# Optimization experiments

Measured on AMD Instinct MI355X. Metric: run time of the kernel, lower is better.

Reference implementation:

```python
import jax, jax.numpy as jnp
import numpy as np

B, T, C, K, TNEI = 16, 1024, 1024, 8, 2
H = int(C * 1.5)  # FeedForward hidden = int(1.5*in_dim)
EPS = 1e-5


def setup_inputs() -> dict:
    key = jax.random.key(0)
    ks = jax.random.split(key, 16)
    ws = C ** -0.5  # fan-in style init scale for projections
    return {
        "x": jax.random.normal(ks[0], (B, T, C), jnp.float32),
        "radj": jax.random.uniform(ks[1], (B, T, K), jnp.float32),
        "inxs": jax.random.randint(ks[2], (B, T, K), 0, T),
        "Wq": jax.random.normal(ks[3], (C, C), jnp.float32) * ws,
        "Wk": jax.random.normal(ks[4], (C, C), jnp.float32) * ws,
        "Wv": jax.random.normal(ks[5], (C, C), jnp.float32) * ws,
        "Wo": jax.random.normal(ks[6], (C, C), jnp.float32) * ws,
        "ln1_g": jnp.ones((C,), jnp.float32),
        "ln1_b": jnp.zeros((C,), jnp.float32),
        "W1": jax.random.normal(ks[7], (C, H), jnp.float32) * ws,
        "b1": jnp.zeros((H,), jnp.float32),
        "W2": jax.random.normal(ks[8], (H, C), jnp.float32) * (H ** -0.5),
        "b2": jnp.zeros((C,), jnp.float32),
        "ln2_g": jnp.ones((C,), jnp.float32),
        "ln2_b": jnp.zeros((C,), jnp.float32),
    }


def _layernorm(x, g, b):
    mu = jnp.mean(x, axis=-1, keepdims=True)
    var = jnp.mean(jnp.square(x - mu), axis=-1, keepdims=True)
    return (x - mu) * jax.lax.rsqrt(var + EPS) * g + b


def reference(x, radj, inxs, Wq, Wk, Wv, Wo, ln1_g, ln1_b, W1, b1, W2, b2, ln2_g, ln2_b):
    scale = 1.0 / jnp.sqrt(jnp.asarray(C, x.dtype))
    gather = jax.vmap(lambda a, i: a[i])  # (T,C),(T,K) -> (T,K,C), vmapped over B

    # MBasicReason: tnei hops of top-k neighbor attention (adjacency-biased)
    h = x
    for _ in range(TNEI):
        q = h @ Wq                                  # (B,T,C)
        kn = gather(h @ Wk, inxs)                   # (B,T,K,C)
        vn = gather(h @ Wv, inxs)                   # (B,T,K,C)
        scores = jnp.einsum('btc,btkc->btk', q, kn) * scale + radj
        attn = jax.nn.softmax(scores, axis=-1)      # (B,T,K); dropout off (eval)
        h = jnp.einsum('btk,btkc->btc', attn, vn) @ Wo

    # residual + LN, FFN, residual + LN
    y = _layernorm(x + jax.nn.relu(h), ln1_g, ln1_b)
    f = jax.nn.relu(y @ W1 + b1) @ W2 + b2
    return _layernorm(y + f, ln2_g, ln2_b)
```

## Files before the change

### kernel.cpp

```cpp
#include <hip/hip_runtime.h>
#include <hip/hip_bf16.h>
#include <cstddef>
#include <cstdint>

#define B_    16
#define T_    1024
#define C_    1024
#define K_    8
#define H_    1536
#define TNEI_ 2
static constexpr float EPS_ = 1e-5f;

typedef __attribute__((ext_vector_type(8))) short bf16x8;
typedef __attribute__((ext_vector_type(4))) float f32x4;

__device__ __forceinline__ float bf2f(unsigned short u) {
    return __uint_as_float(((unsigned)u) << 16);
}
__device__ __forceinline__ unsigned short f2bf(float f) {
    __hip_bfloat16 h = __float2bfloat16(f);
    union { __hip_bfloat16 h; unsigned short u; } cvt;
    cvt.h = h;
    return cvt.u;
}

__device__ __forceinline__ void gload_lds16(const void* g, void* l) {
    __builtin_amdgcn_global_load_lds(
        (const __attribute__((address_space(1))) void*)g,
        (__attribute__((address_space(3))) void*)l,
        16, 0, 0);
}

#define VMCNT0 asm volatile("s_waitcnt vmcnt(0)" ::: "memory")
#define VMCNT4 asm volatile("s_waitcnt vmcnt(4)" ::: "memory")
#define BARRIER do {                                   \
    __builtin_amdgcn_sched_barrier(0);                 \
    __builtin_amdgcn_s_barrier();                      \
    asm volatile("" ::: "memory");                     \
    __builtin_amdgcn_sched_barrier(0);                 \
} while (0)

__global__ __launch_bounds__(256) void f2bf_kernel(
    const float* __restrict__ in, unsigned short* __restrict__ out)
{
    const size_t i = (size_t)blockIdx.x * 256 + threadIdx.x;
    const float4 v = *reinterpret_cast<const float4*>(&in[i * 4]);
    ushort4 o;
    o.x = f2bf(v.x); o.y = f2bf(v.y); o.z = f2bf(v.z); o.w = f2bf(v.w);
    *reinterpret_cast<ushort4*>(&out[i * 4]) = o;
}

__global__ __launch_bounds__(256) void wtrans_kernel(
    const float* __restrict__ W, unsigned short* __restrict__ WT, int R, int Cc)
{
    __shared__ float t[32][33];
    const int c0 = blockIdx.x * 32, r0 = blockIdx.y * 32;
    const int tx = threadIdx.x & 31, ty = threadIdx.x >> 5;
    #pragma unroll
    for (int i = 0; i < 4; ++i)
        t[ty + 8 * i][tx] = W[(size_t)(r0 + ty + 8 * i) * Cc + c0 + tx];
    __syncthreads();
    #pragma unroll
    for (int i = 0; i < 4; ++i)
        WT[(size_t)(c0 + ty + 8 * i) * R + r0 + tx] = f2bf(t[tx][ty + 8 * i]);
}

template <int OUT_BF16, int BIAS, int RELU>
__global__ __launch_bounds__(256, 2) void gemm_bt_kernel(
    const unsigned short* __restrict__ A, const unsigned short* __restrict__ Bt,
    const float* __restrict__ bias, void* __restrict__ Cout,
    int M, int N, int K)
{
    constexpr int BK = 32;
    __shared__ unsigned short smem[3 * 8192];

    const int tid  = threadIdx.x;
    const int lane = tid & 63;
    const int wid  = tid >> 6;
    const int wm   = wid >> 1, wn = wid & 1;

    const int nwg  = gridDim.x * gridDim.y;
    int bidl = blockIdx.y * gridDim.x + blockIdx.x;
    bidl = (bidl & 7) * (nwg >> 3) + (bidl >> 3);
    const int bx = bidl % gridDim.x;
    const int by = bidl / gridDim.x;
    const int row0 = by * 128;
    const int col0 = bx * 128;

    const int NT = K >> 5;

    const int sub = lane >> 2;
    const int kk  = (((lane & 3) ^ ((lane >> 3) & 3))) * 8;

    f32x4 acc[4][4] = {};

    auto stage = [&](int kt, int bufi) {
        unsigned short* As = smem + bufi * 8192;
        unsigned short* Bs = As + 4096;
        #pragma unroll
        for (int i = 0; i < 2; ++i) {
            const int chunk = i * 4 + wid;
            const int r = chunk * 16 + sub;
            gload_lds16(&A[(size_t)(row0 + r) * K + kt + kk], &As[chunk * 512]);
        }
        #pragma unroll
        for (int i = 0; i < 2; ++i) {
            const int chunk = i * 4 + wid;
            const int r = chunk * 16 + sub;
            gload_lds16(&Bt[(size_t)(col0 + r) * K + kt + kk], &Bs[chunk * 512]);
        }
    };

    const int slot = ((lane >> 4) ^ ((lane >> 1) & 3)) * 8;
    auto loadfrag = [&](int bufi, bf16x8* a, bf16x8* b) {
        const unsigned short* As = smem + bufi * 8192;
        const unsigned short* Bs = As + 4096;
        #pragma unroll
        for (int m = 0; m < 4; ++m) {
            const int r = wm * 64 + m * 16 + (lane & 15);
            a[m] = *reinterpret_cast<const bf16x8*>(&As[r * 32 + slot]);
        }
        #pragma unroll
        for (int n = 0; n < 4; ++n) {
            const int c = wn * 64 + n * 16 + (lane & 15);
            b[n] = *reinterpret_cast<const bf16x8*>(&Bs[c * 32 + slot]);
        }
    };

    auto mfma16 = [&](const bf16x8* a, const bf16x8* b) {
        __builtin_amdgcn_s_setprio(1);
        #pragma unroll
        for (int m = 0; m < 4; ++m)
            #pragma unroll
            for (int n = 0; n < 4; ++n)
                acc[m][n] = __builtin_amdgcn_mfma_f32_16x16x32_bf16(
                    a[m], b[n], acc[m][n], 0, 0, 0);
        __builtin_amdgcn_s_setprio(0);
    };

    bf16x8 fa[4], fb[4];

    stage(0, 0);
    stage(BK, 1);
    VMCNT4;
    BARRIER;
    loadfrag(0, fa, fb);

    int bs = 2, br = 1;
    for (int t = 0; t < NT; ++t) {
        if (t + 2 < NT) stage((t + 2) * BK, bs);
        if (++bs == 3) bs = 0;
        mfma16(fa, fb);
        if (t + 1 < NT) {
            if (t + 2 < NT) { VMCNT4; } else { VMCNT0; }
            BARRIER;
            loadfrag(br, fa, fb);
        }
        if (++br == 3) br = 0;
    }

    if (OUT_BF16) {
        __syncthreads();
        char* tile = (char*)smem;
        #pragma unroll
        for (int m = 0; m < 4; ++m) {
            #pragma unroll
            for (int n = 0; n < 4; ++n) {
                const int cc = wn * 64 + n * 16 + (lane & 15);
                const float bv = BIAS ? bias[col0 + cc] : 0.0f;
                #pragma unroll
                for (int r = 0; r < 4; ++r) {
                    const int rr = wm * 64 + m * 16 + (lane >> 4) * 4 + r;
                    float v = acc[m][n][r] + bv;
                    if (RELU) v = fmaxf(v, 0.0f);
                    const int byte = (rr * 256 + cc * 2) ^ (((rr >> 2) & 3) << 5);
                    *reinterpret_cast<unsigned short*>(tile + byte) = f2bf(v);
                }
            }
        }
        __syncthreads();
        const int cchunk = tid & 15;
        const int rloc   = tid >> 4;
        #pragma unroll
        for (int p = 0; p < 8; ++p) {
            const int rr = p * 16 + rloc;
            const int byte = (rr * 256 + cchunk * 16) ^ (((rr >> 2) & 3) << 5);
            const uint4 v = *reinterpret_cast<const uint4*>(tile + byte);
            *reinterpret_cast<uint4*>(
                &((unsigned short*)Cout)[(size_t)(row0 + rr) * N + col0 + cchunk * 8]) = v;
        }
    } else {
        #pragma unroll
        for (int m = 0; m < 4; ++m) {
            #pragma unroll
            for (int n = 0; n < 4; ++n) {
                const int cg = col0 + wn * 64 + n * 16 + (lane & 15);
                const float bv = BIAS ? bias[cg] : 0.0f;
                #pragma unroll
                for (int r = 0; r < 4; ++r) {
                    const int rg = row0 + wm * 64 + m * 16 + (lane >> 4) * 4 + r;
                    float v = acc[m][n][r] + bv;
                    if (RELU) v = fmaxf(v, 0.0f);
                    ((float*)Cout)[(size_t)rg * N + cg] = v;
                }
            }
        }
    }
}

__global__ __launch_bounds__(256) void attn_kernel(
    const unsigned short* __restrict__ qkv, const int* __restrict__ inxs,
    const float* __restrict__ radj, unsigned short* __restrict__ out)
{
    const int bt  = blockIdx.x;
    const int b   = bt >> 10;
    const int tid = threadIdx.x;
    const float scale = 0.03125f;

    __shared__ int   s_idx[K_];
    __shared__ float s_sc[K_];
    __shared__ float red[K_][4];

    if (tid < K_) s_idx[tid] = inxs[bt * K_ + tid];
    __syncthreads();

    const ushort4 qv = *reinterpret_cast<const ushort4*>(
        &qkv[(size_t)bt * 3072 + tid * 4]);
    const float qf[4] = { bf2f(qv.x), bf2f(qv.y), bf2f(qv.z), bf2f(qv.w) };

    float part[K_];
    #pragma unroll
    for (int k = 0; k < K_; ++k) {
        const size_t nb = (size_t)b * T_ + s_idx[k];
        const ushort4 kv = *reinterpret_cast<const ushort4*>(
            &qkv[nb * 3072 + 1024 + tid * 4]);
        part[k] = qf[0] * bf2f(kv.x) + qf[1] * bf2f(kv.y)
                + qf[2] * bf2f(kv.z) + qf[3] * bf2f(kv.w);
    }

    const int lane = tid & 63, wid = tid >> 6;
    #pragma unroll
    for (int k = 0; k < K_; ++k) {
        float v = part[k];
        #pragma unroll
        for (int off = 32; off; off >>= 1) v += __shfl_xor(v, off);
        if (lane == 0) red[k][wid] = v;
    }
    __syncthreads();
    if (tid < K_) {
        s_sc[tid] = (red[tid][0] + red[tid][1] + red[tid][2] + red[tid][3]) * scale
                    + radj[bt * K_ + tid];
    }
    __syncthreads();

    float m = s_sc[0];
    #pragma unroll
    for (int k = 1; k < K_; ++k) m = fmaxf(m, s_sc[k]);
    float w[K_], wsum = 0.f;
    #pragma unroll
    for (int k = 0; k < K_; ++k) { w[k] = expf(s_sc[k] - m); wsum += w[k]; }
    const float inv = 1.0f / wsum;

    float o[4] = {0.f, 0.f, 0.f, 0.f};
    #pragma unroll
    for (int k = 0; k < K_; ++k) {
        const size_t nb = (size_t)b * T_ + s_idx[k];
        const ushort4 vv = *reinterpret_cast<const ushort4*>(
            &qkv[nb * 3072 + 2048 + tid * 4]);
        const float wk = w[k] * inv;
        o[0] = fmaf(wk, bf2f(vv.x), o[0]);
        o[1] = fmaf(wk, bf2f(vv.y), o[1]);
        o[2] = fmaf(wk, bf2f(vv.z), o[2]);
        o[3] = fmaf(wk, bf2f(vv.w), o[3]);
    }
    ushort4 ov;
    ov.x = f2bf(o[0]); ov.y = f2bf(o[1]); ov.z = f2bf(o[2]); ov.w = f2bf(o[3]);
    *reinterpret_cast<ushort4*>(&out[(size_t)bt * C_ + tid * 4]) = ov;
}

template <int RELU, int WB>
__global__ __launch_bounds__(256) void ln_residual_kernel(
    const float* __restrict__ a, const float* __restrict__ bb,
    const float* __restrict__ g, const float* __restrict__ beta,
    float* __restrict__ out, unsigned short* __restrict__ outb)
{
    const int bt  = blockIdx.x;
    const int tid = threadIdx.x;

    const float4 av = *reinterpret_cast<const float4*>(&a[(size_t)bt * C_ + tid * 4]);
    const float4 bv = *reinterpret_cast<const float4*>(&bb[(size_t)bt * C_ + tid * 4]);
    float4 s;
    s.x = av.x + (RELU ? fmaxf(bv.x, 0.f) : bv.x);
    s.y = av.y + (RELU ? fmaxf(bv.y, 0.f) : bv.y);
    s.z = av.z + (RELU ? fmaxf(bv.z, 0.f) : bv.z);
    s.w = av.w + (RELU ? fmaxf(bv.w, 0.f) : bv.w);

    float sum = s.x + s.y + s.z + s.w;
    float sq  = s.x * s.x + s.y * s.y + s.z * s.z + s.w * s.w;

    const int lane = tid & 63, wid = tid >> 6;
    __shared__ float rs[4], rq[4];
    #pragma unroll
    for (int off = 32; off; off >>= 1) {
        sum += __shfl_xor(sum, off);
        sq  += __shfl_xor(sq,  off);
    }
    if (lane == 0) { rs[wid] = sum; rq[wid] = sq; }
    __syncthreads();
    sum = rs[0] + rs[1] + rs[2] + rs[3];
    sq  = rq[0] + rq[1] + rq[2] + rq[3];

    const float mu  = sum * (1.0f / C_);
    const float var = sq * (1.0f / C_) - mu * mu;
    const float r   = rsqrtf(var + EPS_);

    const float4 gv = *reinterpret_cast<const float4*>(&g[tid * 4]);
    const float4 be = *reinterpret_cast<const float4*>(&beta[tid * 4]);
    float4 o;
    o.x = (s.x - mu) * r * gv.x + be.x;
    o.y = (s.y - mu) * r * gv.y + be.y;
    o.z = (s.z - mu) * r * gv.z + be.z;
    o.w = (s.w - mu) * r * gv.w + be.w;
    *reinterpret_cast<float4*>(&out[(size_t)bt * C_ + tid * 4]) = o;
    if (WB) {
        ushort4 ob;
        ob.x = f2bf(o.x); ob.y = f2bf(o.y); ob.z = f2bf(o.z); ob.w = f2bf(o.w);
        *reinterpret_cast<ushort4*>(&outb[(size_t)bt * C_ + tid * 4]) = ob;
    }
}

extern "C" void kernel_launch(void* const* d_in, const int* in_sizes, int n_in,
                              void* d_out, int out_size, void* d_ws, size_t ws_size,
                              hipStream_t stream)
{
    const float* x     = (const float*)d_in[0];
    const float* radj  = (const float*)d_in[1];
    const int*   inxs  = (const int*)  d_in[2];
    const float* Wq    = (const float*)d_in[3];
    const float* Wk    = (const float*)d_in[4];
    const float* Wv    = (const float*)d_in[5];
    const float* Wo    = (const float*)d_in[6];
    const float* ln1_g = (const float*)d_in[7];
    const float* ln1_b = (const float*)d_in[8];
    const float* W1    = (const float*)d_in[9];
    const float* b1    = (const float*)d_in[10];
    const float* W2    = (const float*)d_in[11];
    const float* b2    = (const float*)d_in[12];
    const float* ln2_g = (const float*)d_in[13];
    const float* ln2_b = (const float*)d_in[14];
    float* out = (float*)d_out;

    char* wsb = (char*)d_ws;
    const size_t MB = 1 << 20;
    unsigned short* WqkvT = (unsigned short*)(wsb + 0 * MB);
    unsigned short* WoT   = (unsigned short*)(wsb + 6 * MB);
    unsigned short* W1T   = (unsigned short*)(wsb + 8 * MB);
    unsigned short* W2T   = (unsigned short*)(wsb + 11 * MB);
    unsigned short* xb  = (unsigned short*)(wsb + 16 * MB);
    unsigned short* hb  = xb;
    unsigned short* qkv = (unsigned short*)(wsb + 48 * MB);
    unsigned short* ab  = (unsigned short*)(wsb + 144 * MB);
    float*          h2  = (float*)(wsb + 48 * MB);
    float*          y   = (float*)(wsb + 112 * MB);
    unsigned short* yb  = (unsigned short*)(wsb + 176 * MB);
    unsigned short* hid = (unsigned short*)(wsb + 208 * MB);
    float*          f   = (float*)(wsb + 48 * MB);

    const int M = B_ * T_;
    const dim3 blk(256);
    const dim3 gQKV(3 * C_ / 128, M / 128);
    const dim3 gC(C_ / 128, M / 128);
    const dim3 gH(H_ / 128, M / 128);

    wtrans_kernel<<<dim3(32, 32), blk, 0, stream>>>(Wq, WqkvT,                C_, C_);
    wtrans_kernel<<<dim3(32, 32), blk, 0, stream>>>(Wk, WqkvT + 1024 * 1024,  C_, C_);
    wtrans_kernel<<<dim3(32, 32), blk, 0, stream>>>(Wv, WqkvT + 2048 * 1024,  C_, C_);
    wtrans_kernel<<<dim3(32, 32), blk, 0, stream>>>(Wo, WoT, C_, C_);
    wtrans_kernel<<<dim3(48, 32), blk, 0, stream>>>(W1, W1T, C_, H_);
    wtrans_kernel<<<dim3(32, 48), blk, 0, stream>>>(W2, W2T, H_, C_);
    f2bf_kernel<<<dim3((size_t)M * C_ / 1024), blk, 0, stream>>>(x, xb);

    for (int hop = 0; hop < TNEI_; ++hop) {
        const unsigned short* hin = (hop == 0) ? xb : hb;
        gemm_bt_kernel<1, 0, 0><<<gQKV, blk, 0, stream>>>(hin, WqkvT, nullptr, qkv,
                                                          M, 3 * C_, C_);
        attn_kernel<<<dim3(M), blk, 0, stream>>>(qkv, inxs, radj, ab);
        if (hop == 0)
            gemm_bt_kernel<1, 0, 0><<<gC, blk, 0, stream>>>(ab, WoT, nullptr, hb,
                                                            M, C_, C_);
        else
            gemm_bt_kernel<0, 0, 0><<<gC, blk, 0, stream>>>(ab, WoT, nullptr, h2,
                                                            M, C_, C_);
    }

    ln_residual_kernel<1, 1><<<dim3(M), blk, 0, stream>>>(x, h2, ln1_g, ln1_b, y, yb);
    gemm_bt_kernel<1, 1, 1><<<gH, blk, 0, stream>>>(yb,  W1T, b1, hid, M, H_, C_);
    gemm_bt_kernel<0, 1, 0><<<gC, blk, 0, stream>>>(hid, W2T, b2, f,   M, C_, H_);
    ln_residual_kernel<0, 0><<<dim3(M), blk, 0, stream>>>(y, f, ln2_g, ln2_b, out, nullptr);
}
```

Baseline: 801.8 us.

## Enlarge GEMM tiles to 256x256 with 512-thread workgroups

Doubles the GEMM macro-tile in both dimensions to 256x256 and uses 8 waves per workgroup, each computing a 128x64 sub-tile with twice the accumulators. The bf16 epilogue is reorganised into two passes through LDS so the larger output tile fits the staging buffer. The goal is higher arithmetic intensity and fewer global loads per FLOP. The costs are more registers per thread, larger LDS use, and fewer workgroups, for example only 256 for the C-wide GEMMs, which may hurt occupancy and load balance across CUs.

```diff
diff --git a/kernel.cpp b/kernel.cpp
--- a/kernel.cpp
+++ b/kernel.cpp
@@ -66,58 +66,58 @@
 }
 
 template <int OUT_BF16, int BIAS, int RELU>
-__global__ __launch_bounds__(256, 2) void gemm_bt_kernel(
+__global__ __launch_bounds__(512, 2) void gemm_bt_kernel(
     const unsigned short* __restrict__ A, const unsigned short* __restrict__ Bt,
     const float* __restrict__ bias, void* __restrict__ Cout,
     int M, int N, int K)
 {
     constexpr int BK = 32;
-    __shared__ unsigned short smem[3 * 8192];
+    __shared__ unsigned short smem[3 * 16384];
 
     const int tid  = threadIdx.x;
     const int lane = tid & 63;
     const int wid  = tid >> 6;
-    const int wm   = wid >> 1, wn = wid & 1;
+    const int wm   = wid >> 2, wn = wid & 3;
 
     const int nwg  = gridDim.x * gridDim.y;
     int bidl = blockIdx.y * gridDim.x + blockIdx.x;
     bidl = (bidl & 7) * (nwg >> 3) + (bidl >> 3);
     const int bx = bidl % gridDim.x;
     const int by = bidl / gridDim.x;
-    const int row0 = by * 128;
-    const int col0 = bx * 128;
+    const int row0 = by * 256;
+    const int col0 = bx * 256;
 
     const int NT = K >> 5;
 
     const int sub = lane >> 2;
     const int kk  = (((lane & 3) ^ ((lane >> 3) & 3))) * 8;
 
-    f32x4 acc[4][4] = {};
+    f32x4 acc[8][4] = {};
 
     auto stage = [&](int kt, int bufi) {
-        unsigned short* As = smem + bufi * 8192;
-        unsigned short* Bs = As + 4096;
+        unsigned short* As = smem + bufi * 16384;
+        unsigned short* Bs = As + 8192;
         #pragma unroll
         for (int i = 0; i < 2; ++i) {
-            const int chunk = i * 4 + wid;
-            const int r = chunk * 16 + sub;
-            gload_lds16(&A[(size_t)(row0 + r) * K + kt + kk], &As[chunk * 512]);
+            const int cg = i * 8 + wid;
+            const int r = cg * 16 + sub;
+            gload_lds16(&A[(size_t)(row0 + r) * K + kt + kk], &As[cg * 512]);
         }
         #pragma unroll
         for (int i = 0; i < 2; ++i) {
-            const int chunk = i * 4 + wid;
-            const int r = chunk * 16 + sub;
-            gload_lds16(&Bt[(size_t)(col0 + r) * K + kt + kk], &Bs[chunk * 512]);
+            const int cg = i * 8 + wid;
+            const int r = cg * 16 + sub;
+            gload_lds16(&Bt[(size_t)(col0 + r) * K + kt + kk], &Bs[cg * 512]);
         }
     };
 
     const int slot = ((lane >> 4) ^ ((lane >> 1) & 3)) * 8;
     auto loadfrag = [&](int bufi, bf16x8* a, bf16x8* b) {
-        const unsigned short* As = smem + bufi * 8192;
-        const unsigned short* Bs = As + 4096;
-        #pragma unroll
-        for (int m = 0; m < 4; ++m) {
-            const int r = wm * 64 + m * 16 + (lane & 15);
+        const unsigned short* As = smem + bufi * 16384;
+        const unsigned short* Bs = As + 8192;
+        #pragma unroll
+        for (int m = 0; m < 8; ++m) {
+            const int r = wm * 128 + m * 16 + (lane & 15);
             a[m] = *reinterpret_cast<const bf16x8*>(&As[r * 32 + slot]);
         }
         #pragma unroll
@@ -127,10 +127,10 @@
         }
     };
 
-    auto mfma16 = [&](const bf16x8* a, const bf16x8* b) {
+    auto mfma32 = [&](const bf16x8* a, const bf16x8* b) {
         __builtin_amdgcn_s_setprio(1);
         #pragma unroll
-        for (int m = 0; m < 4; ++m)
+        for (int m = 0; m < 8; ++m)
             #pragma unroll
             for (int n = 0; n < 4; ++n)
                 acc[m][n] = __builtin_amdgcn_mfma_f32_16x16x32_bf16(
@@ -138,7 +138,7 @@
         __builtin_amdgcn_s_setprio(0);
     };
 
-    bf16x8 fa[4], fb[4];
+    bf16x8 fa[8], fb[4];
 
     stage(0, 0);
     stage(BK, 1);
@@ -150,7 +150,7 @@
     for (int t = 0; t < NT; ++t) {
         if (t + 2 < NT) stage((t + 2) * BK, bs);
         if (++bs == 3) bs = 0;
-        mfma16(fa, fb);
+        mfma32(fa, fb);
         if (t + 1 < NT) {
             if (t + 2 < NT) { VMCNT4; } else { VMCNT0; }
             BARRIER;
@@ -160,45 +160,50 @@
     }
 
     if (OUT_BF16) {
-        __syncthreads();
         char* tile = (char*)smem;
         #pragma unroll
-        for (int m = 0; m < 4; ++m) {
+        for (int p = 0; p < 2; ++p) {
+            __syncthreads();
             #pragma unroll
-            for (int n = 0; n < 4; ++n) {
-                const int cc = wn * 64 + n * 16 + (lane & 15);
-                const float bv = BIAS ? bias[col0 + cc] : 0.0f;
+            for (int m4 = 0; m4 < 4; ++m4) {
+                const int m = p * 4 + m4;
                 #pragma unroll
-                for (int r = 0; r < 4; ++r) {
-                    const int rr = wm * 64 + m * 16 + (lane >> 4) * 4 + r;
-                    float v = acc[m][n][r] + bv;
-                    if (RELU) v = fmaxf(v, 0.0f);
-                    const int byte = (rr * 256 + cc * 2) ^ (((rr >> 2) & 3) << 5);
-                    *reinterpret_cast<unsigned short*>(tile + byte) = f2bf(v);
+                for (int n = 0; n < 4; ++n) {
+                    const int cc = wn * 64 + n * 16 + (lane & 15);
+                    const float bv = BIAS ? bias[col0 + cc] : 0.0f;
+                    #pragma unroll
+                    for (int r = 0; r < 4; ++r) {
+                        const int lrow = wm * 64 + m4 * 16 + (lane >> 4) * 4 + r;
+                        float v = acc[m][n][r] + bv;
+                        if (RELU) v = fmaxf(v, 0.0f);
+                        const int byte = (lrow * 512 + cc * 2) ^ (((lrow >> 2) & 3) << 5);
+                        *reinterpret_cast<unsigned short*>(tile + byte) = f2bf(v);
+                    }
                 }
             }
-        }
-        __syncthreads();
-        const int cchunk = tid & 15;
-        const int rloc   = tid >> 4;
-        #pragma unroll
-        for (int p = 0; p < 8; ++p) {
-            const int rr = p * 16 + rloc;
-            const int byte = (rr * 256 + cchunk * 16) ^ (((rr >> 2) & 3) << 5);
-            const uint4 v = *reinterpret_cast<const uint4*>(tile + byte);
-            *reinterpret_cast<uint4*>(
-                &((unsigned short*)Cout)[(size_t)(row0 + rr) * N + col0 + cchunk * 8]) = v;
+            __syncthreads();
+            const int cchunk = tid & 31;
+            const int rbase  = tid >> 5;
+            #pragma unroll
+            for (int it = 0; it < 8; ++it) {
+                const int lr = it * 16 + rbase;
+                const int byte = (lr * 512 + cchunk * 16) ^ (((lr >> 2) & 3) << 5);
+                const uint4 v = *reinterpret_cast<const uint4*>(tile + byte);
+                const int grow = row0 + (lr >> 6) * 128 + p * 64 + (lr & 63);
+                *reinterpret_cast<uint4*>(
+                    &((unsigned short*)Cout)[(size_t)grow * N + col0 + cchunk * 8]) = v;
+            }
         }
     } else {
         #pragma unroll
-        for (int m = 0; m < 4; ++m) {
+        for (int m = 0; m < 8; ++m) {
             #pragma unroll
             for (int n = 0; n < 4; ++n) {
                 const int cg = col0 + wn * 64 + n * 16 + (lane & 15);
                 const float bv = BIAS ? bias[cg] : 0.0f;
                 #pragma unroll
                 for (int r = 0; r < 4; ++r) {
-                    const int rg = row0 + wm * 64 + m * 16 + (lane >> 4) * 4 + r;
+                    const int rg = row0 + wm * 128 + m * 16 + (lane >> 4) * 4 + r;
                     float v = acc[m][n][r] + bv;
                     if (RELU) v = fmaxf(v, 0.0f);
                     ((float*)Cout)[(size_t)rg * N + cg] = v;
@@ -368,9 +373,10 @@
 
     const int M = B_ * T_;
     const dim3 blk(256);
-    const dim3 gQKV(3 * C_ / 128, M / 128);
-    const dim3 gC(C_ / 128, M / 128);
-    const dim3 gH(H_ / 128, M / 128);
+    const dim3 blkG(512);
+    const dim3 gQKV(3 * C_ / 256, M / 256);
+    const dim3 gC(C_ / 256, M / 256);
+    const dim3 gH(H_ / 256, M / 256);
 
     wtrans_kernel<<<dim3(32, 32), blk, 0, stream>>>(Wq, WqkvT,                C_, C_);
     wtrans_kernel<<<dim3(32, 32), blk, 0, stream>>>(Wk, WqkvT + 1024 * 1024,  C_, C_);
@@ -382,19 +388,19 @@
 
     for (int hop = 0; hop < TNEI_; ++hop) {
         const unsigned short* hin = (hop == 0) ? xb : hb;
-        gemm_bt_kernel<1, 0, 0><<<gQKV, blk, 0, stream>>>(hin, WqkvT, nullptr, qkv,
-                                                          M, 3 * C_, C_);
+        gemm_bt_kernel<1, 0, 0><<<gQKV, blkG, 0, stream>>>(hin, WqkvT, nullptr, qkv,
+                                                           M, 3 * C_, C_);
         attn_kernel<<<dim3(M), blk, 0, stream>>>(qkv, inxs, radj, ab);
         if (hop == 0)
-            gemm_bt_kernel<1, 0, 0><<<gC, blk, 0, stream>>>(ab, WoT, nullptr, hb,
-                                                            M, C_, C_);
+            gemm_bt_kernel<1, 0, 0><<<gC, blkG, 0, stream>>>(ab, WoT, nullptr, hb,
+                                                             M, C_, C_);
         else
-            gemm_bt_kernel<0, 0, 0><<<gC, blk, 0, stream>>>(ab, WoT, nullptr, h2,
-                                                            M, C_, C_);
+            gemm_bt_kernel<0, 0, 0><<<gC, blkG, 0, stream>>>(ab, WoT, nullptr, h2,
+                                                             M, C_, C_);
     }
 
     ln_residual_kernel<1, 1><<<dim3(M), blk, 0, stream>>>(x, h2, ln1_g, ln1_b, y, yb);
-    gemm_bt_kernel<1, 1, 1><<<gH, blk, 0, stream>>>(yb,  W1T, b1, hid, M, H_, C_);
-    gemm_bt_kernel<0, 1, 0><<<gC, blk, 0, stream>>>(hid, W2T, b2, f,   M, C_, H_);
+    gemm_bt_kernel<1, 1, 1><<<gH, blkG, 0, stream>>>(yb,  W1T, b1, hid, M, H_, C_);
+    gemm_bt_kernel<0, 1, 0><<<gC, blkG, 0, stream>>>(hid, W2T, b2, f,   M, C_, H_);
     ln_residual_kernel<0, 0><<<dim3(M), blk, 0, stream>>>(y, f, ln2_g, ln2_b, out, nullptr);
 }
```

Measured after the change: 789.6 us. About the same (-1.5%).
